# Kernel tuning notes

Hardware: AMD Instinct MI355X
Metric: run time of the kernel (lower is better)

The kernel has to match this reference:

```python
import jax, jax.numpy as jnp
import numpy as np

N = 100000          # number of active sparse points
GRID = 800          # coordinate grid extent (2D)
KS = 9              # 3x3 kernel offsets
C_IN = 24
C_HID = 144         # round(24 * 6)
C_OUT = 24
EPS = 1e-5


def _build_kernel_map():
    """Build MinkowskiEngine-style kernel map for a 3x3 stride-1 channelwise conv.
    Returns (in_idx, out_idx, off_id), each [KS*N] int32. Invalid (no neighbor)
    entries point to sentinel row N so the padded gather/scatter is a no-op."""
    rng = np.random.default_rng(0)
    flat = rng.choice(GRID * GRID, size=N, replace=False)  # unique 2D coords
    ys, xs = flat // GRID, flat % GRID
    coord_to_idx = -np.ones(GRID * GRID, dtype=np.int64)
    coord_to_idx[flat] = np.arange(N)
    in_chunks, out_chunks, off_chunks = [], [], []
    pts = np.arange(N, dtype=np.int64)
    k = 0
    for dy in (-1, 0, 1):
        for dx in (-1, 0, 1):
            ny, nx = ys + dy, xs + dx
            inside = (ny >= 0) & (ny < GRID) & (nx >= 0) & (nx < GRID)
            nflat = np.clip(ny, 0, GRID - 1) * GRID + np.clip(nx, 0, GRID - 1)
            nidx = np.where(inside, coord_to_idx[nflat], -1)
            valid = nidx >= 0
            in_chunks.append(np.where(valid, nidx, N))
            out_chunks.append(np.where(valid, pts, N))
            off_chunks.append(np.full(N, k, dtype=np.int64))
            k += 1
    in_idx = np.concatenate(in_chunks).astype(np.int32)
    out_idx = np.concatenate(out_chunks).astype(np.int32)
    off_id = np.concatenate(off_chunks).astype(np.int32)
    return in_idx, out_idx, off_id


def setup_inputs() -> dict:
    key = jax.random.key(0)
    ks = jax.random.split(key, 4)
    in_idx, out_idx, off_id = _build_kernel_map()
    return {
        "feats": jax.random.normal(ks[0], (N, C_IN), jnp.float32),
        "w1": jax.random.normal(ks[1], (C_IN, C_HID), jnp.float32) * 0.1,
        "g1": jnp.ones((C_HID,), jnp.float32),
        "b1": jnp.zeros((C_HID,), jnp.float32),
        "w2": jax.random.normal(ks[2], (KS, C_HID), jnp.float32) * 0.1,
        "g2": jnp.ones((C_HID,), jnp.float32),
        "b2": jnp.zeros((C_HID,), jnp.float32),
        "w3": jax.random.normal(ks[3], (C_HID, C_OUT), jnp.float32) * 0.1,
        "g3": jnp.ones((C_OUT,), jnp.float32),
        "b3": jnp.zeros((C_OUT,), jnp.float32),
        "in_idx": jnp.asarray(in_idx),
        "out_idx": jnp.asarray(out_idx),
        "off_id": jnp.asarray(off_id),
    }


def _bn(x, g, b):
    # MinkowskiBatchNorm forward (training mode): per-channel stats over points
    m = jnp.mean(x, axis=0)
    v = jnp.var(x, axis=0)
    return (x - m) * jax.lax.rsqrt(v + EPS) * g + b


def _relu6(x):
    return jnp.clip(x, 0.0, 6.0)


def _channelwise_conv3x3(x, w2, in_idx, out_idx, off_id):
    # gather-multiply-scatter: out[p, c] = sum_k w2[k, c] * x[nbr_k(p), c]
    xp = jnp.concatenate([x, jnp.zeros((1, x.shape[1]), x.dtype)], axis=0)  # sentinel row
    contrib = xp[in_idx] * w2[off_id]                     # [KS*N, C_HID]
    out = jnp.zeros((N + 1, x.shape[1]), x.dtype).at[out_idx].add(contrib)
    return out[:N]


def reference(feats, w1, g1, b1, w2, g2, b2, w3, g3, b3, in_idx, out_idx, off_id):
    x = _relu6(_bn(feats @ w1, g1, b1))                   # 1x1 expand
    x = _relu6(_bn(_channelwise_conv3x3(x, w2, in_idx, out_idx, off_id), g2, b2))
    x = _bn(x @ w3, g3, b3)                               # 1x1 project
    return x + feats                                      # residual (in==out, stride==1)
```

## Files before the change

kernel.cpp:

```cpp
#include <hip/hip_runtime.h>
#include <hip/hip_fp16.h>

#define N_PTS 100000
#define KSZ 9
#define C_IN 24
#define C_HID 144
#define C_OUT 24
#define G4_HID 36
#define G8_HID 18
#define G4_OUT 6
#define EPSV 1e-5f

#define X2H_B     28800288
#define SENT_B    28800000
#define Y3F_O     14400072
#define ST_O      16800072
#define ST_B      67200288
#define MU1_O     (ST_O + 0)
#define M1_O      (ST_O + 32)
#define SUM2_O    (ST_O + 640)
#define SQ2_O     (ST_O + 800)
#define SUM3_O    (ST_O + 960)
#define SQ3_O     (ST_O + 992)

__device__ inline float4 f4z() { return make_float4(0.f, 0.f, 0.f, 0.f); }
__device__ inline float4 f4_add(float4 a, float4 b) {
    return make_float4(a.x + b.x, a.y + b.y, a.z + b.z, a.w + b.w);
}
__device__ inline float4 f4_fma4(float4 a, float4 b, float4 c) {
    return make_float4(fmaf(a.x, b.x, c.x), fmaf(a.y, b.y, c.y),
                       fmaf(a.z, b.z, c.z), fmaf(a.w, b.w, c.w));
}
__device__ inline float4 f4_fma_s(float s, float4 b, float4 c) {
    return make_float4(fmaf(s, b.x, c.x), fmaf(s, b.y, c.y),
                       fmaf(s, b.z, c.z), fmaf(s, b.w, c.w));
}
__device__ inline float4 f4_clamp6(float4 a) {
    return make_float4(fminf(fmaxf(a.x, 0.f), 6.f), fminf(fmaxf(a.y, 0.f), 6.f),
                       fminf(fmaxf(a.z, 0.f), 6.f), fminf(fmaxf(a.w, 0.f), 6.f));
}
__device__ inline unsigned pack2(float a, float b) {
    __half2 h = __floats2half2_rn(a, b);
    return *reinterpret_cast<unsigned*>(&h);
}
__device__ inline float2 uph(unsigned u) {
    __half2 h = *reinterpret_cast<__half2*>(&u);
    return __half22float2(h);
}

#define MROWS 128
__device__ inline float task_acc(const float* tile, int cnt, int task) {
    if (task < 576) {
        int i = task / 24, j = task % 24;
        float a = 0.f;
        for (int r = 0; r < cnt; r++) a += tile[r * 24 + i] * tile[r * 24 + j];
        return a;
    }
    int k = task - 576;
    float a = 0.f;
    for (int r = 0; r < cnt; r++) a += tile[r * 24 + k];
    return a;
}
__global__ __launch_bounds__(256) void k_moments(const float* __restrict__ feats,
                                                 float* __restrict__ ws) {
    __shared__ float tile[MROWS * C_IN];
    int t = threadIdx.x;
    float acc0 = 0.f, acc1 = 0.f, acc2 = 0.f;
    int nChunks = (N_PTS + MROWS - 1) / MROWS;
    for (int ch = blockIdx.x; ch < nChunks; ch += gridDim.x) {
        int r0 = ch * MROWS;
        int cnt = min(MROWS, N_PTS - r0);
        __syncthreads();
        for (int e = t; e < cnt * C_IN; e += 256) tile[e] = feats[(size_t)r0 * C_IN + e];
        __syncthreads();
        acc0 += task_acc(tile, cnt, t);
        acc1 += task_acc(tile, cnt, t + 256);
        if (t < 88) acc2 += task_acc(tile, cnt, t + 512);
    }
    atomicAdd(&ws[M1_O + t], acc0);
    atomicAdd(&ws[M1_O + t + 256], acc1);
    if (t < 88) {
        int task = t + 512;
        if (task < 576) atomicAdd(&ws[M1_O + task], acc2);
        else            atomicAdd(&ws[MU1_O + task - 576], acc2);
    }
}

__global__ __launch_bounds__(256) void k_gemm1(const float* __restrict__ feats,
                                               const float* __restrict__ w1,
                                               const float* __restrict__ g1,
                                               const float* __restrict__ b1,
                                               float* __restrict__ ws) {
    __shared__ float4 w1s[C_IN * G4_HID];
    __shared__ float M1s[576];
    __shared__ float MU1s[24];
    __shared__ float scf[C_HID], shf[C_HID];
    int t = threadIdx.x;
    for (int e = t; e < C_IN * G4_HID; e += 256) w1s[e] = ((const float4*)w1)[e];
    for (int e = t; e < 576; e += 256) M1s[e] = ws[M1_O + e];
    if (t < 24) MU1s[t] = ws[MU1_O + t];
    __syncthreads();
    if (t < C_HID) {
        const float* w1f = (const float*)w1s;
        float wc[C_IN];
#pragma unroll
        for (int k = 0; k < C_IN; k++) wc[k] = w1f[k * C_HID + t];
        const float invN = 1.f / (float)N_PTS;
        float mean = 0.f;
#pragma unroll
        for (int k = 0; k < C_IN; k++) mean += MU1s[k] * wc[k];
        mean *= invN;
        float e2 = 0.f;
        for (int i = 0; i < C_IN; i++) {
            float s = 0.f;
#pragma unroll
            for (int j = 0; j < C_IN; j++) s += M1s[i * 24 + j] * wc[j];
            e2 += wc[i] * s;
        }
        e2 *= invN;
        float var = e2 - mean * mean;
        float s1 = g1[t] * rsqrtf(var + EPSV);
        scf[t] = s1;
        shf[t] = b1[t] - mean * s1;
    }
    __syncthreads();
    const float4* sc4 = (const float4*)scf;
    const float4* sh4 = (const float4*)shf;
    uint4* x1u = (uint4*)ws;
    const int T = N_PTS * G8_HID;
    for (int tau = blockIdx.x * 256 + t; tau < T; tau += gridDim.x * 256) {
        int p = tau / G8_HID;
        int g = tau % G8_HID;
        const float4* fr = (const float4*)(feats + (size_t)p * C_IN);
        float4 a0 = f4z(), a1 = f4z();
#pragma unroll
        for (int q = 0; q < 6; q++) {
            float4 fq = fr[q];
            a0 = f4_fma_s(fq.x, w1s[(4 * q + 0) * G4_HID + 2 * g], a0);
            a1 = f4_fma_s(fq.x, w1s[(4 * q + 0) * G4_HID + 2 * g + 1], a1);
            a0 = f4_fma_s(fq.y, w1s[(4 * q + 1) * G4_HID + 2 * g], a0);
            a1 = f4_fma_s(fq.y, w1s[(4 * q + 1) * G4_HID + 2 * g + 1], a1);
            a0 = f4_fma_s(fq.z, w1s[(4 * q + 2) * G4_HID + 2 * g], a0);
            a1 = f4_fma_s(fq.z, w1s[(4 * q + 2) * G4_HID + 2 * g + 1], a1);
            a0 = f4_fma_s(fq.w, w1s[(4 * q + 3) * G4_HID + 2 * g], a0);
            a1 = f4_fma_s(fq.w, w1s[(4 * q + 3) * G4_HID + 2 * g + 1], a1);
        }
        a0 = f4_clamp6(f4_fma4(a0, sc4[2 * g], sh4[2 * g]));
        a1 = f4_clamp6(f4_fma4(a1, sc4[2 * g + 1], sh4[2 * g + 1]));
        uint4 o;
        o.x = pack2(a0.x, a0.y); o.y = pack2(a0.z, a0.w);
        o.z = pack2(a1.x, a1.y); o.w = pack2(a1.z, a1.w);
        x1u[tau] = o;
    }
}

__global__ __launch_bounds__(256, 6) void k_conv(const float* __restrict__ w2,
                                                 const int* __restrict__ in_idx,
                                                 float* __restrict__ ws) {
    __shared__ float4 w2s[KSZ * G4_HID];
    __shared__ float lsum[C_HID], lsq[C_HID];
    int t = threadIdx.x;
    for (int e = t; e < KSZ * G4_HID; e += 256) w2s[e] = ((const float4*)w2)[e];
    if (t < C_HID) { lsum[t] = 0.f; lsq[t] = 0.f; }
    __syncthreads();
    const uint4* x1u = (const uint4*)ws;
    uint4* x2u = (uint4*)((char*)ws + X2H_B);
    bool active = t < 252;
    int pt = t / G8_HID, g = t % G8_HID;
    float4 rsA = f4z(), rsB = f4z(), rqA = f4z(), rqB = f4z();
    int nChunks = (N_PTS + 13) / 14;
    for (int ch = blockIdx.x; ch < nChunks; ch += gridDim.x) {
        int p = ch * 14 + pt;
        if (active && p < N_PTS) {
            int idx[KSZ];
#pragma unroll
            for (int k = 0; k < KSZ; k++) idx[k] = in_idx[k * N_PTS + p];
            float4 aA = f4z(), aB = f4z();
#pragma unroll
            for (int k = 0; k < KSZ; k++) {
                uint4 v = x1u[(size_t)idx[k] * G8_HID + g];
                float2 f0 = uph(v.x), f1 = uph(v.y), f2 = uph(v.z), f3 = uph(v.w);
                aA = f4_fma4(w2s[k * G4_HID + 2 * g], make_float4(f0.x, f0.y, f1.x, f1.y), aA);
                aB = f4_fma4(w2s[k * G4_HID + 2 * g + 1], make_float4(f2.x, f2.y, f3.x, f3.y), aB);
            }
            uint4 o;
            o.x = pack2(aA.x, aA.y); o.y = pack2(aA.z, aA.w);
            o.z = pack2(aB.x, aB.y); o.w = pack2(aB.z, aB.w);
            x2u[(size_t)p * G8_HID + g] = o;
            rsA = f4_add(rsA, aA); rsB = f4_add(rsB, aB);
            rqA = f4_fma4(aA, aA, rqA); rqB = f4_fma4(aB, aB, rqB);
        }
    }
    if (active) {
        int c0 = 8 * g;
        atomicAdd(&lsum[c0 + 0], rsA.x); atomicAdd(&lsum[c0 + 1], rsA.y);
        atomicAdd(&lsum[c0 + 2], rsA.z); atomicAdd(&lsum[c0 + 3], rsA.w);
        atomicAdd(&lsum[c0 + 4], rsB.x); atomicAdd(&lsum[c0 + 5], rsB.y);
        atomicAdd(&lsum[c0 + 6], rsB.z); atomicAdd(&lsum[c0 + 7], rsB.w);
        atomicAdd(&lsq[c0 + 0], rqA.x);  atomicAdd(&lsq[c0 + 1], rqA.y);
        atomicAdd(&lsq[c0 + 2], rqA.z);  atomicAdd(&lsq[c0 + 3], rqA.w);
        atomicAdd(&lsq[c0 + 4], rqB.x);  atomicAdd(&lsq[c0 + 5], rqB.y);
        atomicAdd(&lsq[c0 + 6], rqB.z);  atomicAdd(&lsq[c0 + 7], rqB.w);
    }
    __syncthreads();
    if (t < C_HID) {
        atomicAdd(&ws[SUM2_O + t], lsum[t]);
        atomicAdd(&ws[SQ2_O + t], lsq[t]);
    }
}

#define TP 64
__global__ __launch_bounds__(256) void k_gemm2(const float* __restrict__ w3,
                                               const float* __restrict__ g2,
                                               const float* __restrict__ b2,
                                               float* __restrict__ ws) {
    __shared__ float xs[TP * 145];
    __shared__ float w3s[C_HID * C_OUT];
    __shared__ float sc2s[C_HID], sh2s[C_HID];
    __shared__ float ssum[C_OUT], ssq[C_OUT];
    int t = threadIdx.x;
    for (int e = t; e < C_HID * C_OUT / 4; e += 256)
        ((float4*)w3s)[e] = ((const float4*)w3)[e];
    if (t < C_HID) {
        const float invN = 1.f / (float)N_PTS;
        float mean = ws[SUM2_O + t] * invN;
        float var = ws[SQ2_O + t] * invN - mean * mean;
        float s = g2[t] * rsqrtf(var + EPSV);
        sc2s[t] = s;
        sh2s[t] = b2[t] - mean * s;
    }
    if (t < C_OUT) { ssum[t] = 0.f; ssq[t] = 0.f; }
    __syncthreads();
    const uint4* x2u = (const uint4*)((char*)ws + X2H_B);
    int p0 = blockIdx.x * TP;
    for (int e = t; e < TP * G8_HID; e += 256) {
        int row = e / G8_HID, col = e % G8_HID;
        int p = p0 + row;
        int c0 = 8 * col;
        float v[8];
        if (p < N_PTS) {
            uint4 u = x2u[(size_t)p * G8_HID + col];
            float2 f0 = uph(u.x), f1 = uph(u.y), f2 = uph(u.z), f3 = uph(u.w);
            v[0] = f0.x; v[1] = f0.y; v[2] = f1.x; v[3] = f1.y;
            v[4] = f2.x; v[5] = f2.y; v[6] = f3.x; v[7] = f3.y;
#pragma unroll
            for (int i = 0; i < 8; i++)
                v[i] = fminf(fmaxf(fmaf(v[i], sc2s[c0 + i], sh2s[c0 + i]), 0.f), 6.f);
        } else {
#pragma unroll
            for (int i = 0; i < 8; i++) v[i] = 0.f;
        }
#pragma unroll
        for (int i = 0; i < 8; i++) xs[row * 145 + c0 + i] = v[i];
    }
    __syncthreads();
    int pl = t & 63, cg = t >> 6;
    int c0 = 6 * cg;
    float acc[6] = {0.f, 0.f, 0.f, 0.f, 0.f, 0.f};
    const float* xr = xs + pl * 145;
#pragma unroll 4
    for (int h = 0; h < C_HID; h++) {
        float x = xr[h];
#pragma unroll
        for (int j = 0; j < 6; j++) acc[j] = fmaf(x, w3s[h * C_OUT + c0 + j], acc[j]);
    }
    int p = p0 + pl;
    bool valid = p < N_PTS;
    float* y3 = ws + Y3F_O;
    if (valid) {
#pragma unroll
        for (int j = 0; j < 6; j++) y3[(size_t)p * C_OUT + c0 + j] = acc[j];
    }
    float s[6], q[6];
#pragma unroll
    for (int j = 0; j < 6; j++) {
        s[j] = valid ? acc[j] : 0.f;
        q[j] = s[j] * s[j];
    }
#pragma unroll
    for (int off = 32; off > 0; off >>= 1) {
#pragma unroll
        for (int j = 0; j < 6; j++) {
            s[j] += __shfl_down(s[j], off);
            q[j] += __shfl_down(q[j], off);
        }
    }
    if (pl == 0) {
#pragma unroll
        for (int j = 0; j < 6; j++) {
            atomicAdd(&ssum[c0 + j], s[j]);
            atomicAdd(&ssq[c0 + j], q[j]);
        }
    }
    __syncthreads();
    if (t < C_OUT) {
        atomicAdd(&ws[SUM3_O + t], ssum[t]);
        atomicAdd(&ws[SQ3_O + t], ssq[t]);
    }
}

__global__ __launch_bounds__(256) void k_out(const float* __restrict__ feats,
                                             const float* __restrict__ g3,
                                             const float* __restrict__ b3,
                                             const float* __restrict__ ws,
                                             float* __restrict__ out) {
    __shared__ float scs[C_OUT], shs[C_OUT];
    int t = threadIdx.x;
    if (t < C_OUT) {
        const float invN = 1.f / (float)N_PTS;
        float mean = ws[SUM3_O + t] * invN;
        float var = ws[SQ3_O + t] * invN - mean * mean;
        float s = g3[t] * rsqrtf(var + EPSV);
        scs[t] = s;
        shs[t] = b3[t] - mean * s;
    }
    __syncthreads();
    int t4 = blockIdx.x * 256 + t;
    const int T = N_PTS * G4_OUT;
    if (t4 >= T) return;
    int g = t4 % G4_OUT;
    float4 y = ((const float4*)(ws + Y3F_O))[t4];
    float4 s = ((const float4*)scs)[g];
    float4 b = ((const float4*)shs)[g];
    float4 f = ((const float4*)feats)[t4];
    ((float4*)out)[t4] = f4_add(f4_fma4(y, s, b), f);
}

extern "C" void kernel_launch(void* const* d_in, const int* in_sizes, int n_in,
                              void* d_out, int out_size, void* d_ws, size_t ws_size,
                              hipStream_t stream) {
    const float* feats = (const float*)d_in[0];
    const float* w1 = (const float*)d_in[1];
    const float* g1 = (const float*)d_in[2];
    const float* b1 = (const float*)d_in[3];
    const float* w2 = (const float*)d_in[4];
    const float* g2 = (const float*)d_in[5];
    const float* b2 = (const float*)d_in[6];
    const float* w3 = (const float*)d_in[7];
    const float* g3 = (const float*)d_in[8];
    const float* b3 = (const float*)d_in[9];
    const int* in_idx = (const int*)d_in[10];
    float* ws = (float*)d_ws;
    float* out = (float*)d_out;

    hipMemsetAsync((char*)d_ws + ST_B, 0, 4096, stream);
    hipMemsetAsync((char*)d_ws + SENT_B, 0, 288, stream);

    hipLaunchKernelGGL(k_moments, dim3(256), dim3(256), 0, stream, feats, ws);
    hipLaunchKernelGGL(k_gemm1, dim3(512), dim3(256), 0, stream, feats, w1, g1, b1, ws);
    hipLaunchKernelGGL(k_conv, dim3(2048), dim3(256), 0, stream, w2, in_idx, ws);
    hipLaunchKernelGGL(k_gemm2, dim3((N_PTS + TP - 1) / TP), dim3(256), 0, stream,
                       w3, g2, b2, ws);
    hipLaunchKernelGGL(k_out, dim3((N_PTS * G4_OUT + 255) / 256), dim3(256), 0, stream,
                       feats, g3, b3, ws, out);
}
```

Before: 312.9 us.

## Fuse all five stages into one cooperative persistent kernel with grid syncs

Replaces the two memsets and five kernel launches with a single cooperative kernel that runs each stage in turn, separated by grid-wide barriers, and zeroes the stats buffers inside the kernel. The conv stage now keeps its weights in registers instead of shared memory. The gemm2 stage stages activations in shared memory as half2 to shrink the tile. This removes launch gaps and per-kernel setup, but costs grid-sync overhead, a grid limited to what can be resident at once, and extra fp16 rounding in the gemm2 tile.

```diff
diff --git a/kernel.cpp b/kernel.cpp
--- a/kernel.cpp
+++ b/kernel.cpp
@@ -1,5 +1,8 @@
 #include <hip/hip_runtime.h>
 #include <hip/hip_fp16.h>
+#include <hip/hip_cooperative_groups.h>
+
+namespace cg = cooperative_groups;
 
 #define N_PTS 100000
 #define KSZ 9
@@ -12,10 +15,8 @@
 #define EPSV 1e-5f
 
 #define X2H_B     28800288
-#define SENT_B    28800000
 #define Y3F_O     14400072
 #define ST_O      16800072
-#define ST_B      67200288
 #define MU1_O     (ST_O + 0)
 #define M1_O      (ST_O + 32)
 #define SUM2_O    (ST_O + 640)
@@ -61,269 +62,304 @@
     for (int r = 0; r < cnt; r++) a += tile[r * 24 + k];
     return a;
 }
-__global__ __launch_bounds__(256) void k_moments(const float* __restrict__ feats,
-                                                 float* __restrict__ ws) {
-    __shared__ float tile[MROWS * C_IN];
-    int t = threadIdx.x;
-    float acc0 = 0.f, acc1 = 0.f, acc2 = 0.f;
-    int nChunks = (N_PTS + MROWS - 1) / MROWS;
-    for (int ch = blockIdx.x; ch < nChunks; ch += gridDim.x) {
-        int r0 = ch * MROWS;
-        int cnt = min(MROWS, N_PTS - r0);
-        __syncthreads();
-        for (int e = t; e < cnt * C_IN; e += 256) tile[e] = feats[(size_t)r0 * C_IN + e];
-        __syncthreads();
-        acc0 += task_acc(tile, cnt, t);
-        acc1 += task_acc(tile, cnt, t + 256);
-        if (t < 88) acc2 += task_acc(tile, cnt, t + 512);
-    }
-    atomicAdd(&ws[M1_O + t], acc0);
-    atomicAdd(&ws[M1_O + t + 256], acc1);
-    if (t < 88) {
-        int task = t + 512;
-        if (task < 576) atomicAdd(&ws[M1_O + task], acc2);
-        else            atomicAdd(&ws[MU1_O + task - 576], acc2);
-    }
-}
-
-__global__ __launch_bounds__(256) void k_gemm1(const float* __restrict__ feats,
-                                               const float* __restrict__ w1,
-                                               const float* __restrict__ g1,
-                                               const float* __restrict__ b1,
-                                               float* __restrict__ ws) {
-    __shared__ float4 w1s[C_IN * G4_HID];
-    __shared__ float M1s[576];
-    __shared__ float MU1s[24];
-    __shared__ float scf[C_HID], shf[C_HID];
-    int t = threadIdx.x;
-    for (int e = t; e < C_IN * G4_HID; e += 256) w1s[e] = ((const float4*)w1)[e];
-    for (int e = t; e < 576; e += 256) M1s[e] = ws[M1_O + e];
-    if (t < 24) MU1s[t] = ws[MU1_O + t];
-    __syncthreads();
-    if (t < C_HID) {
-        const float* w1f = (const float*)w1s;
-        float wc[C_IN];
-#pragma unroll
-        for (int k = 0; k < C_IN; k++) wc[k] = w1f[k * C_HID + t];
-        const float invN = 1.f / (float)N_PTS;
-        float mean = 0.f;
-#pragma unroll
-        for (int k = 0; k < C_IN; k++) mean += MU1s[k] * wc[k];
-        mean *= invN;
-        float e2 = 0.f;
-        for (int i = 0; i < C_IN; i++) {
-            float s = 0.f;
-#pragma unroll
-            for (int j = 0; j < C_IN; j++) s += M1s[i * 24 + j] * wc[j];
-            e2 += wc[i] * s;
-        }
-        e2 *= invN;
-        float var = e2 - mean * mean;
-        float s1 = g1[t] * rsqrtf(var + EPSV);
-        scf[t] = s1;
-        shf[t] = b1[t] - mean * s1;
-    }
-    __syncthreads();
-    const float4* sc4 = (const float4*)scf;
-    const float4* sh4 = (const float4*)shf;
-    uint4* x1u = (uint4*)ws;
-    const int T = N_PTS * G8_HID;
-    for (int tau = blockIdx.x * 256 + t; tau < T; tau += gridDim.x * 256) {
-        int p = tau / G8_HID;
-        int g = tau % G8_HID;
-        const float4* fr = (const float4*)(feats + (size_t)p * C_IN);
-        float4 a0 = f4z(), a1 = f4z();
-#pragma unroll
-        for (int q = 0; q < 6; q++) {
-            float4 fq = fr[q];
-            a0 = f4_fma_s(fq.x, w1s[(4 * q + 0) * G4_HID + 2 * g], a0);
-            a1 = f4_fma_s(fq.x, w1s[(4 * q + 0) * G4_HID + 2 * g + 1], a1);
-            a0 = f4_fma_s(fq.y, w1s[(4 * q + 1) * G4_HID + 2 * g], a0);
-            a1 = f4_fma_s(fq.y, w1s[(4 * q + 1) * G4_HID + 2 * g + 1], a1);
-            a0 = f4_fma_s(fq.z, w1s[(4 * q + 2) * G4_HID + 2 * g], a0);
-            a1 = f4_fma_s(fq.z, w1s[(4 * q + 2) * G4_HID + 2 * g + 1], a1);
-            a0 = f4_fma_s(fq.w, w1s[(4 * q + 3) * G4_HID + 2 * g], a0);
-            a1 = f4_fma_s(fq.w, w1s[(4 * q + 3) * G4_HID + 2 * g + 1], a1);
-        }
-        a0 = f4_clamp6(f4_fma4(a0, sc4[2 * g], sh4[2 * g]));
-        a1 = f4_clamp6(f4_fma4(a1, sc4[2 * g + 1], sh4[2 * g + 1]));
-        uint4 o;
-        o.x = pack2(a0.x, a0.y); o.y = pack2(a0.z, a0.w);
-        o.z = pack2(a1.x, a1.y); o.w = pack2(a1.z, a1.w);
-        x1u[tau] = o;
-    }
-}
-
-__global__ __launch_bounds__(256, 6) void k_conv(const float* __restrict__ w2,
-                                                 const int* __restrict__ in_idx,
-                                                 float* __restrict__ ws) {
-    __shared__ float4 w2s[KSZ * G4_HID];
-    __shared__ float lsum[C_HID], lsq[C_HID];
-    int t = threadIdx.x;
-    for (int e = t; e < KSZ * G4_HID; e += 256) w2s[e] = ((const float4*)w2)[e];
-    if (t < C_HID) { lsum[t] = 0.f; lsq[t] = 0.f; }
-    __syncthreads();
-    const uint4* x1u = (const uint4*)ws;
-    uint4* x2u = (uint4*)((char*)ws + X2H_B);
-    bool active = t < 252;
-    int pt = t / G8_HID, g = t % G8_HID;
-    float4 rsA = f4z(), rsB = f4z(), rqA = f4z(), rqB = f4z();
-    int nChunks = (N_PTS + 13) / 14;
-    for (int ch = blockIdx.x; ch < nChunks; ch += gridDim.x) {
-        int p = ch * 14 + pt;
-        if (active && p < N_PTS) {
-            int idx[KSZ];
-#pragma unroll
-            for (int k = 0; k < KSZ; k++) idx[k] = in_idx[k * N_PTS + p];
-            float4 aA = f4z(), aB = f4z();
-#pragma unroll
-            for (int k = 0; k < KSZ; k++) {
-                uint4 v = x1u[(size_t)idx[k] * G8_HID + g];
-                float2 f0 = uph(v.x), f1 = uph(v.y), f2 = uph(v.z), f3 = uph(v.w);
-                aA = f4_fma4(w2s[k * G4_HID + 2 * g], make_float4(f0.x, f0.y, f1.x, f1.y), aA);
-                aB = f4_fma4(w2s[k * G4_HID + 2 * g + 1], make_float4(f2.x, f2.y, f3.x, f3.y), aB);
-            }
+
+__global__ __launch_bounds__(256, 4) void k_fused(
+    const float* __restrict__ feats, const float* __restrict__ w1,
+    const float* __restrict__ g1, const float* __restrict__ b1,
+    const float* __restrict__ w2, const float* __restrict__ g2,
+    const float* __restrict__ b2, const float* __restrict__ w3,
+    const float* __restrict__ g3, const float* __restrict__ b3,
+    const int* __restrict__ in_idx, float* __restrict__ ws,
+    float* __restrict__ out) {
+    __shared__ __align__(16) char smem[33920];
+    cg::grid_group gg = cg::this_grid();
+    const int t = threadIdx.x;
+    const int bid = blockIdx.x;
+    const int nB = gridDim.x;
+
+    if (bid == 0) {
+        for (int i = t; i < 1024; i += 256) ws[ST_O + i] = 0.f;
+        if (t < G8_HID) {
+            uint4 z; z.x = 0u; z.y = 0u; z.z = 0u; z.w = 0u;
+            ((uint4*)ws)[(size_t)N_PTS * G8_HID + t] = z;
+        }
+    }
+    gg.sync();
+
+    {
+        float* tile = (float*)smem;
+        float acc0 = 0.f, acc1 = 0.f, acc2 = 0.f;
+        const int nChunks = (N_PTS + MROWS - 1) / MROWS;
+        for (int ch = bid; ch < nChunks; ch += nB) {
+            int r0 = ch * MROWS;
+            int cnt = min(MROWS, N_PTS - r0);
+            __syncthreads();
+            for (int e = t; e < cnt * C_IN; e += 256)
+                tile[e] = feats[(size_t)r0 * C_IN + e];
+            __syncthreads();
+            acc0 += task_acc(tile, cnt, t);
+            acc1 += task_acc(tile, cnt, t + 256);
+            if (t < 88) acc2 += task_acc(tile, cnt, t + 512);
+        }
+        if (bid < nChunks) {
+            atomicAdd(&ws[M1_O + t], acc0);
+            atomicAdd(&ws[M1_O + t + 256], acc1);
+            if (t < 88) {
+                int task = t + 512;
+                if (task < 576) atomicAdd(&ws[M1_O + task], acc2);
+                else            atomicAdd(&ws[MU1_O + task - 576], acc2);
+            }
+        }
+    }
+    gg.sync();
+
+    {
+        float4* w1s = (float4*)smem;
+        float*  M1s = (float*)(smem + 13824);
+        float*  MU1s = (float*)(smem + 16128);
+        float*  scf = (float*)(smem + 16224);
+        float*  shf = (float*)(smem + 16800);
+        for (int e = t; e < C_IN * G4_HID; e += 256) w1s[e] = ((const float4*)w1)[e];
+        for (int e = t; e < 576; e += 256) M1s[e] = ws[M1_O + e];
+        if (t < 24) MU1s[t] = ws[MU1_O + t];
+        __syncthreads();
+        if (t < C_HID) {
+            const float* w1f = (const float*)w1s;
+            float wc[C_IN];
+#pragma unroll
+            for (int k = 0; k < C_IN; k++) wc[k] = w1f[k * C_HID + t];
+            const float invN = 1.f / (float)N_PTS;
+            float mean = 0.f;
+#pragma unroll
+            for (int k = 0; k < C_IN; k++) mean += MU1s[k] * wc[k];
+            mean *= invN;
+            float e2 = 0.f;
+            for (int i = 0; i < C_IN; i++) {
+                float s = 0.f;
+#pragma unroll
+                for (int j = 0; j < C_IN; j++) s += M1s[i * 24 + j] * wc[j];
+                e2 += wc[i] * s;
+            }
+            e2 *= invN;
+            float var = e2 - mean * mean;
+            float s1 = g1[t] * rsqrtf(var + EPSV);
+            scf[t] = s1;
+            shf[t] = b1[t] - mean * s1;
+        }
+        __syncthreads();
+        const float4* sc4 = (const float4*)scf;
+        const float4* sh4 = (const float4*)shf;
+        uint4* x1u = (uint4*)ws;
+        const int T = N_PTS * G8_HID;
+        for (int tau = bid * 256 + t; tau < T; tau += nB * 256) {
+            int p = tau / G8_HID;
+            int g = tau % G8_HID;
+            const float4* fr = (const float4*)(feats + (size_t)p * C_IN);
+            float4 a0 = f4z(), a1 = f4z();
+#pragma unroll
+            for (int q = 0; q < 6; q++) {
+                float4 fq = fr[q];
+                a0 = f4_fma_s(fq.x, w1s[(4 * q + 0) * G4_HID + 2 * g], a0);
+                a1 = f4_fma_s(fq.x, w1s[(4 * q + 0) * G4_HID + 2 * g + 1], a1);
+                a0 = f4_fma_s(fq.y, w1s[(4 * q + 1) * G4_HID + 2 * g], a0);
+                a1 = f4_fma_s(fq.y, w1s[(4 * q + 1) * G4_HID + 2 * g + 1], a1);
+                a0 = f4_fma_s(fq.z, w1s[(4 * q + 2) * G4_HID + 2 * g], a0);
+                a1 = f4_fma_s(fq.z, w1s[(4 * q + 2) * G4_HID + 2 * g + 1], a1);
+                a0 = f4_fma_s(fq.w, w1s[(4 * q + 3) * G4_HID + 2 * g], a0);
+                a1 = f4_fma_s(fq.w, w1s[(4 * q + 3) * G4_HID + 2 * g + 1], a1);
+            }
+            a0 = f4_clamp6(f4_fma4(a0, sc4[2 * g], sh4[2 * g]));
+            a1 = f4_clamp6(f4_fma4(a1, sc4[2 * g + 1], sh4[2 * g + 1]));
             uint4 o;
-            o.x = pack2(aA.x, aA.y); o.y = pack2(aA.z, aA.w);
-            o.z = pack2(aB.x, aB.y); o.w = pack2(aB.z, aB.w);
-            x2u[(size_t)p * G8_HID + g] = o;
-            rsA = f4_add(rsA, aA); rsB = f4_add(rsB, aB);
-            rqA = f4_fma4(aA, aA, rqA); rqB = f4_fma4(aB, aB, rqB);
-        }
-    }
-    if (active) {
-        int c0 = 8 * g;
-        atomicAdd(&lsum[c0 + 0], rsA.x); atomicAdd(&lsum[c0 + 1], rsA.y);
-        atomicAdd(&lsum[c0 + 2], rsA.z); atomicAdd(&lsum[c0 + 3], rsA.w);
-        atomicAdd(&lsum[c0 + 4], rsB.x); atomicAdd(&lsum[c0 + 5], rsB.y);
-        atomicAdd(&lsum[c0 + 6], rsB.z); atomicAdd(&lsum[c0 + 7], rsB.w);
-        atomicAdd(&lsq[c0 + 0], rqA.x);  atomicAdd(&lsq[c0 + 1], rqA.y);
-        atomicAdd(&lsq[c0 + 2], rqA.z);  atomicAdd(&lsq[c0 + 3], rqA.w);
-        atomicAdd(&lsq[c0 + 4], rqB.x);  atomicAdd(&lsq[c0 + 5], rqB.y);
-        atomicAdd(&lsq[c0 + 6], rqB.z);  atomicAdd(&lsq[c0 + 7], rqB.w);
-    }
-    __syncthreads();
-    if (t < C_HID) {
-        atomicAdd(&ws[SUM2_O + t], lsum[t]);
-        atomicAdd(&ws[SQ2_O + t], lsq[t]);
-    }
-}
-
-#define TP 64
-__global__ __launch_bounds__(256) void k_gemm2(const float* __restrict__ w3,
-                                               const float* __restrict__ g2,
-                                               const float* __restrict__ b2,
-                                               float* __restrict__ ws) {
-    __shared__ float xs[TP * 145];
-    __shared__ float w3s[C_HID * C_OUT];
-    __shared__ float sc2s[C_HID], sh2s[C_HID];
-    __shared__ float ssum[C_OUT], ssq[C_OUT];
-    int t = threadIdx.x;
-    for (int e = t; e < C_HID * C_OUT / 4; e += 256)
-        ((float4*)w3s)[e] = ((const float4*)w3)[e];
-    if (t < C_HID) {
-        const float invN = 1.f / (float)N_PTS;
-        float mean = ws[SUM2_O + t] * invN;
-        float var = ws[SQ2_O + t] * invN - mean * mean;
-        float s = g2[t] * rsqrtf(var + EPSV);
-        sc2s[t] = s;
-        sh2s[t] = b2[t] - mean * s;
-    }
-    if (t < C_OUT) { ssum[t] = 0.f; ssq[t] = 0.f; }
-    __syncthreads();
-    const uint4* x2u = (const uint4*)((char*)ws + X2H_B);
-    int p0 = blockIdx.x * TP;
-    for (int e = t; e < TP * G8_HID; e += 256) {
-        int row = e / G8_HID, col = e % G8_HID;
-        int p = p0 + row;
-        int c0 = 8 * col;
-        float v[8];
-        if (p < N_PTS) {
-            uint4 u = x2u[(size_t)p * G8_HID + col];
-            float2 f0 = uph(u.x), f1 = uph(u.y), f2 = uph(u.z), f3 = uph(u.w);
-            v[0] = f0.x; v[1] = f0.y; v[2] = f1.x; v[3] = f1.y;
-            v[4] = f2.x; v[5] = f2.y; v[6] = f3.x; v[7] = f3.y;
-#pragma unroll
-            for (int i = 0; i < 8; i++)
-                v[i] = fminf(fmaxf(fmaf(v[i], sc2s[c0 + i], sh2s[c0 + i]), 0.f), 6.f);
-        } else {
-#pragma unroll
-            for (int i = 0; i < 8; i++) v[i] = 0.f;
-        }
-#pragma unroll
-        for (int i = 0; i < 8; i++) xs[row * 145 + c0 + i] = v[i];
-    }
-    __syncthreads();
-    int pl = t & 63, cg = t >> 6;
-    int c0 = 6 * cg;
-    float acc[6] = {0.f, 0.f, 0.f, 0.f, 0.f, 0.f};
-    const float* xr = xs + pl * 145;
-#pragma unroll 4
-    for (int h = 0; h < C_HID; h++) {
-        float x = xr[h];
-#pragma unroll
-        for (int j = 0; j < 6; j++) acc[j] = fmaf(x, w3s[h * C_OUT + c0 + j], acc[j]);
-    }
-    int p = p0 + pl;
-    bool valid = p < N_PTS;
-    float* y3 = ws + Y3F_O;
-    if (valid) {
-#pragma unroll
-        for (int j = 0; j < 6; j++) y3[(size_t)p * C_OUT + c0 + j] = acc[j];
-    }
-    float s[6], q[6];
-#pragma unroll
-    for (int j = 0; j < 6; j++) {
-        s[j] = valid ? acc[j] : 0.f;
-        q[j] = s[j] * s[j];
-    }
-#pragma unroll
-    for (int off = 32; off > 0; off >>= 1) {
-#pragma unroll
-        for (int j = 0; j < 6; j++) {
-            s[j] += __shfl_down(s[j], off);
-            q[j] += __shfl_down(q[j], off);
-        }
-    }
-    if (pl == 0) {
-#pragma unroll
-        for (int j = 0; j < 6; j++) {
-            atomicAdd(&ssum[c0 + j], s[j]);
-            atomicAdd(&ssq[c0 + j], q[j]);
-        }
-    }
-    __syncthreads();
-    if (t < C_OUT) {
-        atomicAdd(&ws[SUM3_O + t], ssum[t]);
-        atomicAdd(&ws[SQ3_O + t], ssq[t]);
-    }
-}
-
-__global__ __launch_bounds__(256) void k_out(const float* __restrict__ feats,
-                                             const float* __restrict__ g3,
-                                             const float* __restrict__ b3,
-                                             const float* __restrict__ ws,
-                                             float* __restrict__ out) {
-    __shared__ float scs[C_OUT], shs[C_OUT];
-    int t = threadIdx.x;
-    if (t < C_OUT) {
-        const float invN = 1.f / (float)N_PTS;
-        float mean = ws[SUM3_O + t] * invN;
-        float var = ws[SQ3_O + t] * invN - mean * mean;
-        float s = g3[t] * rsqrtf(var + EPSV);
-        scs[t] = s;
-        shs[t] = b3[t] - mean * s;
-    }
-    __syncthreads();
-    int t4 = blockIdx.x * 256 + t;
-    const int T = N_PTS * G4_OUT;
-    if (t4 >= T) return;
-    int g = t4 % G4_OUT;
-    float4 y = ((const float4*)(ws + Y3F_O))[t4];
-    float4 s = ((const float4*)scs)[g];
-    float4 b = ((const float4*)shs)[g];
-    float4 f = ((const float4*)feats)[t4];
-    ((float4*)out)[t4] = f4_add(f4_fma4(y, s, b), f);
+            o.x = pack2(a0.x, a0.y); o.y = pack2(a0.z, a0.w);
+            o.z = pack2(a1.x, a1.y); o.w = pack2(a1.z, a1.w);
+            x1u[tau] = o;
+        }
+    }
+    gg.sync();
+
+    {
+        float* lsum = (float*)smem;
+        float* lsq  = (float*)(smem + 576);
+        if (t < C_HID) { lsum[t] = 0.f; lsq[t] = 0.f; }
+        __syncthreads();
+        const uint4* x1u = (const uint4*)ws;
+        uint4* x2u = (uint4*)((char*)ws + X2H_B);
+        bool active = t < 252;
+        int pt = t / G8_HID, g = t % G8_HID;
+        const float4* w2v = (const float4*)w2;
+        float4 wA[KSZ], wB[KSZ];
+#pragma unroll
+        for (int k = 0; k < KSZ; k++) {
+            wA[k] = w2v[k * G4_HID + 2 * g];
+            wB[k] = w2v[k * G4_HID + 2 * g + 1];
+        }
+        float4 rsA = f4z(), rsB = f4z(), rqA = f4z(), rqB = f4z();
+        const int nChunks = (N_PTS + 13) / 14;
+        for (int ch = bid; ch < nChunks; ch += nB) {
+            int p = ch * 14 + pt;
+            if (active && p < N_PTS) {
+                int idx[KSZ];
+#pragma unroll
+                for (int k = 0; k < KSZ; k++) idx[k] = in_idx[k * N_PTS + p];
+                float4 aA = f4z(), aB = f4z();
+#pragma unroll
+                for (int k = 0; k < KSZ; k++) {
+                    uint4 v = x1u[(size_t)idx[k] * G8_HID + g];
+                    float2 f0 = uph(v.x), f1 = uph(v.y), f2 = uph(v.z), f3 = uph(v.w);
+                    aA = f4_fma4(wA[k], make_float4(f0.x, f0.y, f1.x, f1.y), aA);
+                    aB = f4_fma4(wB[k], make_float4(f2.x, f2.y, f3.x, f3.y), aB);
+                }
+                uint4 o;
+                o.x = pack2(aA.x, aA.y); o.y = pack2(aA.z, aA.w);
+                o.z = pack2(aB.x, aB.y); o.w = pack2(aB.z, aB.w);
+                x2u[(size_t)p * G8_HID + g] = o;
+                rsA = f4_add(rsA, aA); rsB = f4_add(rsB, aB);
+                rqA = f4_fma4(aA, aA, rqA); rqB = f4_fma4(aB, aB, rqB);
+            }
+        }
+        if (active) {
+            int c0 = 8 * g;
+            atomicAdd(&lsum[c0 + 0], rsA.x); atomicAdd(&lsum[c0 + 1], rsA.y);
+            atomicAdd(&lsum[c0 + 2], rsA.z); atomicAdd(&lsum[c0 + 3], rsA.w);
+            atomicAdd(&lsum[c0 + 4], rsB.x); atomicAdd(&lsum[c0 + 5], rsB.y);
+            atomicAdd(&lsum[c0 + 6], rsB.z); atomicAdd(&lsum[c0 + 7], rsB.w);
+            atomicAdd(&lsq[c0 + 0], rqA.x);  atomicAdd(&lsq[c0 + 1], rqA.y);
+            atomicAdd(&lsq[c0 + 2], rqA.z);  atomicAdd(&lsq[c0 + 3], rqA.w);
+            atomicAdd(&lsq[c0 + 4], rqB.x);  atomicAdd(&lsq[c0 + 5], rqB.y);
+            atomicAdd(&lsq[c0 + 6], rqB.z);  atomicAdd(&lsq[c0 + 7], rqB.w);
+        }
+        __syncthreads();
+        if (t < C_HID) {
+            atomicAdd(&ws[SUM2_O + t], lsum[t]);
+            atomicAdd(&ws[SQ2_O + t], lsq[t]);
+        }
+    }
+    gg.sync();
+
+    {
+        float*   w3s  = (float*)smem;
+        float*   sc2s = (float*)(smem + 13824);
+        float*   sh2s = (float*)(smem + 14400);
+        float*   ssum = (float*)(smem + 14976);
+        float*   ssq  = (float*)(smem + 15072);
+        __half2* xs2  = (__half2*)(smem + 15168);
+        for (int e = t; e < C_HID * C_OUT / 4; e += 256)
+            ((float4*)w3s)[e] = ((const float4*)w3)[e];
+        if (t < C_HID) {
+            const float invN = 1.f / (float)N_PTS;
+            float mean = ws[SUM2_O + t] * invN;
+            float var = ws[SQ2_O + t] * invN - mean * mean;
+            float s = g2[t] * rsqrtf(var + EPSV);
+            sc2s[t] = s;
+            sh2s[t] = b2[t] - mean * s;
+        }
+        if (t < C_OUT) { ssum[t] = 0.f; ssq[t] = 0.f; }
+        __syncthreads();
+        const uint4* x2u = (const uint4*)((char*)ws + X2H_B);
+        float* y3 = ws + Y3F_O;
+        int pl = t & 63, cgid = t >> 6, c0 = 6 * cgid;
+        const int nTiles = (N_PTS + 63) / 64;
+        for (int tile = bid; tile < nTiles; tile += nB) {
+            int p0 = tile * 64;
+            for (int e = t; e < 64 * G8_HID; e += 256) {
+                int row = e / G8_HID, col = e % G8_HID;
+                int p = p0 + row;
+                float v[8];
+                if (p < N_PTS) {
+                    uint4 u = x2u[(size_t)p * G8_HID + col];
+                    float2 f0 = uph(u.x), f1 = uph(u.y), f2 = uph(u.z), f3 = uph(u.w);
+                    v[0] = f0.x; v[1] = f0.y; v[2] = f1.x; v[3] = f1.y;
+                    v[4] = f2.x; v[5] = f2.y; v[6] = f3.x; v[7] = f3.y;
+                    int cb = 8 * col;
+#pragma unroll
+                    for (int i = 0; i < 8; i++)
+                        v[i] = fminf(fmaxf(fmaf(v[i], sc2s[cb + i], sh2s[cb + i]), 0.f), 6.f);
+                } else {
+#pragma unroll
+                    for (int i = 0; i < 8; i++) v[i] = 0.f;
+                }
+                int base = row * 73 + col * 4;
+                xs2[base + 0] = __floats2half2_rn(v[0], v[1]);
+                xs2[base + 1] = __floats2half2_rn(v[2], v[3]);
+                xs2[base + 2] = __floats2half2_rn(v[4], v[5]);
+                xs2[base + 3] = __floats2half2_rn(v[6], v[7]);
+            }
+            __syncthreads();
+            float acc[6] = {0.f, 0.f, 0.f, 0.f, 0.f, 0.f};
+            const __half2* xr = xs2 + pl * 73;
+#pragma unroll 8
+            for (int hh = 0; hh < 72; hh++) {
+                float2 xv = __half22float2(xr[hh]);
+                int h = 2 * hh;
+#pragma unroll
+                for (int j = 0; j < 6; j++)
+                    acc[j] = fmaf(xv.x, w3s[h * C_OUT + c0 + j], acc[j]);
+#pragma unroll
+                for (int j = 0; j < 6; j++)
+                    acc[j] = fmaf(xv.y, w3s[(h + 1) * C_OUT + c0 + j], acc[j]);
+            }
+            int p = p0 + pl;
+            bool valid = p < N_PTS;
+            if (valid) {
+#pragma unroll
+                for (int j = 0; j < 6; j++) y3[(size_t)p * C_OUT + c0 + j] = acc[j];
+            }
+            float s[6], q[6];
+#pragma unroll
+            for (int j = 0; j < 6; j++) {
+                s[j] = valid ? acc[j] : 0.f;
+                q[j] = s[j] * s[j];
+            }
+#pragma unroll
+            for (int off = 32; off > 0; off >>= 1) {
+#pragma unroll
+                for (int j = 0; j < 6; j++) {
+                    s[j] += __shfl_down(s[j], off);
+                    q[j] += __shfl_down(q[j], off);
+                }
+            }
+            if (pl == 0) {
+#pragma unroll
+                for (int j = 0; j < 6; j++) {
+                    atomicAdd(&ssum[c0 + j], s[j]);
+                    atomicAdd(&ssq[c0 + j], q[j]);
+                }
+            }
+            __syncthreads();
+        }
+        if (bid < nTiles && t < C_OUT) {
+            atomicAdd(&ws[SUM3_O + t], ssum[t]);
+            atomicAdd(&ws[SQ3_O + t], ssq[t]);
+        }
+    }
+    gg.sync();
+
+    {
+        float* scs = (float*)smem;
+        float* shs = (float*)(smem + 128);
+        if (t < C_OUT) {
+            const float invN = 1.f / (float)N_PTS;
+            float mean = ws[SUM3_O + t] * invN;
+            float var = ws[SQ3_O + t] * invN - mean * mean;
+            float s = g3[t] * rsqrtf(var + EPSV);
+            scs[t] = s;
+            shs[t] = b3[t] - mean * s;
+        }
+        __syncthreads();
+        const float4* y3v = (const float4*)(ws + Y3F_O);
+        const float4* fv = (const float4*)feats;
+        float4* ov = (float4*)out;
+        const int T = N_PTS * G4_OUT;
+        for (int e = bid * 256 + t; e < T; e += nB * 256) {
+            int g = e % G4_OUT;
+            float4 y = y3v[e];
+            float4 s = ((const float4*)scs)[g];
+            float4 b = ((const float4*)shs)[g];
+            float4 f = fv[e];
+            ov[e] = f4_add(f4_fma4(y, s, b), f);
+        }
+    }
 }
 
 extern "C" void kernel_launch(void* const* d_in, const int* in_sizes, int n_in,
@@ -343,14 +379,16 @@
     float* ws = (float*)d_ws;
     float* out = (float*)d_out;
 
-    hipMemsetAsync((char*)d_ws + ST_B, 0, 4096, stream);
-    hipMemsetAsync((char*)d_ws + SENT_B, 0, 288, stream);
-
-    hipLaunchKernelGGL(k_moments, dim3(256), dim3(256), 0, stream, feats, ws);
-    hipLaunchKernelGGL(k_gemm1, dim3(512), dim3(256), 0, stream, feats, w1, g1, b1, ws);
-    hipLaunchKernelGGL(k_conv, dim3(2048), dim3(256), 0, stream, w2, in_idx, ws);
-    hipLaunchKernelGGL(k_gemm2, dim3((N_PTS + TP - 1) / TP), dim3(256), 0, stream,
-                       w3, g2, b2, ws);
-    hipLaunchKernelGGL(k_out, dim3((N_PTS * G4_OUT + 255) / 256), dim3(256), 0, stream,
-                       feats, g3, b3, ws, out);
-}
+    void* args[] = {
+        (void*)&feats, (void*)&w1, (void*)&g1, (void*)&b1, (void*)&w2,
+        (void*)&g2, (void*)&b2, (void*)&w3, (void*)&g3, (void*)&b3,
+        (void*)&in_idx, (void*)&ws, (void*)&out};
+
+    int maxB = 2;
+    hipOccupancyMaxActiveBlocksPerMultiprocessor(&maxB, (const void*)k_fused, 256, 0);
+    if (maxB < 1) maxB = 1;
+    int grid = maxB * 256;
+    if (grid > 2048) grid = 2048;
+    hipLaunchCooperativeKernel((const void*)k_fused, dim3(grid), dim3(256),
+                               args, 0, stream);
+}
```

Result: slower. 500.8 us (+60.0%).

## Drop moments kernel; compute BN1 stats in gemm1 and apply BN1 in conv

Applied to the files above, without the earlier changes.

Removes the separate second-moment pass over feats. gemm1 now writes the raw pre-BN expansion in fp16 and accumulates per-channel sum and sum-of-squares. The conv kernel derives the BN1 scale and shift from those stats and applies normalize plus ReLU6 on each gathered neighbor, skipping sentinel indices, so the sentinel-row memset also goes. gemm1 is restructured to use one 64-point tile per block staged through shared memory. In exchange, conv does 9x more BN arithmetic per output and adds a branch per neighbor, and stats are computed from fp32 values while the conv reads fp16-rounded ones.

```diff
diff --git a/kernel.cpp b/kernel.cpp
--- a/kernel.cpp
+++ b/kernel.cpp
@@ -11,17 +11,16 @@
 #define G4_OUT 6
 #define EPSV 1e-5f
 
-#define X2H_B     28800288
-#define SENT_B    28800000
-#define Y3F_O     14400072
-#define ST_O      16800072
-#define ST_B      67200288
-#define MU1_O     (ST_O + 0)
-#define M1_O      (ST_O + 32)
-#define SUM2_O    (ST_O + 640)
-#define SQ2_O     (ST_O + 800)
-#define SUM3_O    (ST_O + 960)
-#define SQ3_O     (ST_O + 992)
+#define X2H_B     28800000
+#define Y3F_O     14400000
+#define ST_O      16800000
+#define ST_B      67200000
+#define SUM1_O    (ST_O + 0)
+#define SQ1_O     (ST_O + 160)
+#define SUM2_O    (ST_O + 320)
+#define SQ2_O     (ST_O + 480)
+#define SUM3_O    (ST_O + 640)
+#define SQ3_O     (ST_O + 672)
 
 __device__ inline float4 f4z() { return make_float4(0.f, 0.f, 0.f, 0.f); }
 __device__ inline float4 f4_add(float4 a, float4 b) {
@@ -48,127 +47,110 @@
     return __half22float2(h);
 }
 
-#define MROWS 128
-__device__ inline float task_acc(const float* tile, int cnt, int task) {
-    if (task < 576) {
-        int i = task / 24, j = task % 24;
-        float a = 0.f;
-        for (int r = 0; r < cnt; r++) a += tile[r * 24 + i] * tile[r * 24 + j];
-        return a;
-    }
-    int k = task - 576;
-    float a = 0.f;
-    for (int r = 0; r < cnt; r++) a += tile[r * 24 + k];
-    return a;
-}
-__global__ __launch_bounds__(256) void k_moments(const float* __restrict__ feats,
-                                                 float* __restrict__ ws) {
-    __shared__ float tile[MROWS * C_IN];
-    int t = threadIdx.x;
-    float acc0 = 0.f, acc1 = 0.f, acc2 = 0.f;
-    int nChunks = (N_PTS + MROWS - 1) / MROWS;
-    for (int ch = blockIdx.x; ch < nChunks; ch += gridDim.x) {
-        int r0 = ch * MROWS;
-        int cnt = min(MROWS, N_PTS - r0);
-        __syncthreads();
-        for (int e = t; e < cnt * C_IN; e += 256) tile[e] = feats[(size_t)r0 * C_IN + e];
-        __syncthreads();
-        acc0 += task_acc(tile, cnt, t);
-        acc1 += task_acc(tile, cnt, t + 256);
-        if (t < 88) acc2 += task_acc(tile, cnt, t + 512);
-    }
-    atomicAdd(&ws[M1_O + t], acc0);
-    atomicAdd(&ws[M1_O + t + 256], acc1);
-    if (t < 88) {
-        int task = t + 512;
-        if (task < 576) atomicAdd(&ws[M1_O + task], acc2);
-        else            atomicAdd(&ws[MU1_O + task - 576], acc2);
-    }
-}
-
 __global__ __launch_bounds__(256) void k_gemm1(const float* __restrict__ feats,
                                                const float* __restrict__ w1,
-                                               const float* __restrict__ g1,
-                                               const float* __restrict__ b1,
                                                float* __restrict__ ws) {
-    __shared__ float4 w1s[C_IN * G4_HID];
-    __shared__ float M1s[576];
-    __shared__ float MU1s[24];
-    __shared__ float scf[C_HID], shf[C_HID];
-    int t = threadIdx.x;
+    __shared__ __align__(16) char smem[38272];
+    float*  xs   = (float*)smem;
+    float4* w1s  = (float4*)(smem + 6400);
+    float*  tile = (float*)smem;
+    float*  lsum = (float*)(smem + 37120);
+    float*  lsq  = (float*)(smem + 37696);
+    const int t = threadIdx.x;
+    const int p0 = blockIdx.x * 64;
     for (int e = t; e < C_IN * G4_HID; e += 256) w1s[e] = ((const float4*)w1)[e];
-    for (int e = t; e < 576; e += 256) M1s[e] = ws[M1_O + e];
-    if (t < 24) MU1s[t] = ws[MU1_O + t];
+    for (int e = t; e < 64 * C_IN; e += 256) {
+        int r = e / C_IN, c = e % C_IN;
+        int p = p0 + r;
+        xs[r * 25 + c] = (p < N_PTS) ? feats[(size_t)p * C_IN + c] : 0.f;
+    }
+    if (t < C_HID) { lsum[t] = 0.f; lsq[t] = 0.f; }
+    __syncthreads();
+    const int pt = t & 63;
+    const int cg = __builtin_amdgcn_readfirstlane(t >> 6);
+    float4 acc[9];
+#pragma unroll
+    for (int j = 0; j < 9; j++) acc[j] = f4z();
+    for (int k = 0; k < C_IN; k++) {
+        float xk = xs[pt * 25 + k];
+        const float4* wr = &w1s[k * G4_HID + cg * 9];
+#pragma unroll
+        for (int j = 0; j < 9; j++) acc[j] = f4_fma_s(xk, wr[j], acc[j]);
+    }
+    __syncthreads();
+    {
+        float* dst = tile + pt * 145 + cg * 36;
+#pragma unroll
+        for (int j = 0; j < 9; j++) {
+            dst[4 * j + 0] = acc[j].x; dst[4 * j + 1] = acc[j].y;
+            dst[4 * j + 2] = acc[j].z; dst[4 * j + 3] = acc[j].w;
+        }
+    }
+    __syncthreads();
+    uint4* y1u = (uint4*)ws;
+    bool active = t < 252;
+    int g = t % G8_HID, r0 = t / G8_HID;
+    float4 rsA = f4z(), rsB = f4z(), rqA = f4z(), rqB = f4z();
+    if (active) {
+        for (int r = r0; r < 64; r += 14) {
+            int p = p0 + r;
+            if (p >= N_PTS) break;
+            const float* src = tile + r * 145 + 8 * g;
+            float v0 = src[0], v1 = src[1], v2 = src[2], v3 = src[3];
+            float v4 = src[4], v5 = src[5], v6 = src[6], v7 = src[7];
+            uint4 o;
+            o.x = pack2(v0, v1); o.y = pack2(v2, v3);
+            o.z = pack2(v4, v5); o.w = pack2(v6, v7);
+            y1u[(size_t)p * G8_HID + g] = o;
+            float4 aA = make_float4(v0, v1, v2, v3), aB = make_float4(v4, v5, v6, v7);
+            rsA = f4_add(rsA, aA); rsB = f4_add(rsB, aB);
+            rqA = f4_fma4(aA, aA, rqA); rqB = f4_fma4(aB, aB, rqB);
+        }
+        int c0 = 8 * g;
+        atomicAdd(&lsum[c0 + 0], rsA.x); atomicAdd(&lsum[c0 + 1], rsA.y);
+        atomicAdd(&lsum[c0 + 2], rsA.z); atomicAdd(&lsum[c0 + 3], rsA.w);
+        atomicAdd(&lsum[c0 + 4], rsB.x); atomicAdd(&lsum[c0 + 5], rsB.y);
+        atomicAdd(&lsum[c0 + 6], rsB.z); atomicAdd(&lsum[c0 + 7], rsB.w);
+        atomicAdd(&lsq[c0 + 0], rqA.x);  atomicAdd(&lsq[c0 + 1], rqA.y);
+        atomicAdd(&lsq[c0 + 2], rqA.z);  atomicAdd(&lsq[c0 + 3], rqA.w);
+        atomicAdd(&lsq[c0 + 4], rqB.x);  atomicAdd(&lsq[c0 + 5], rqB.y);
+        atomicAdd(&lsq[c0 + 6], rqB.z);  atomicAdd(&lsq[c0 + 7], rqB.w);
+    }
     __syncthreads();
     if (t < C_HID) {
-        const float* w1f = (const float*)w1s;
-        float wc[C_IN];
-#pragma unroll
-        for (int k = 0; k < C_IN; k++) wc[k] = w1f[k * C_HID + t];
+        atomicAdd(&ws[SUM1_O + t], lsum[t]);
+        atomicAdd(&ws[SQ1_O + t], lsq[t]);
+    }
+}
+
+__global__ __launch_bounds__(256) void k_conv(const float* __restrict__ w2,
+                                              const float* __restrict__ g1,
+                                              const float* __restrict__ b1,
+                                              const int* __restrict__ in_idx,
+                                              float* __restrict__ ws) {
+    __shared__ float4 w2s[KSZ * G4_HID];
+    __shared__ float sc1L[C_HID], sh1L[C_HID];
+    __shared__ float lsum[C_HID], lsq[C_HID];
+    const int t = threadIdx.x;
+    for (int e = t; e < KSZ * G4_HID; e += 256) w2s[e] = ((const float4*)w2)[e];
+    if (t < C_HID) {
         const float invN = 1.f / (float)N_PTS;
-        float mean = 0.f;
-#pragma unroll
-        for (int k = 0; k < C_IN; k++) mean += MU1s[k] * wc[k];
-        mean *= invN;
-        float e2 = 0.f;
-        for (int i = 0; i < C_IN; i++) {
-            float s = 0.f;
-#pragma unroll
-            for (int j = 0; j < C_IN; j++) s += M1s[i * 24 + j] * wc[j];
-            e2 += wc[i] * s;
-        }
-        e2 *= invN;
-        float var = e2 - mean * mean;
-        float s1 = g1[t] * rsqrtf(var + EPSV);
-        scf[t] = s1;
-        shf[t] = b1[t] - mean * s1;
-    }
-    __syncthreads();
-    const float4* sc4 = (const float4*)scf;
-    const float4* sh4 = (const float4*)shf;
-    uint4* x1u = (uint4*)ws;
-    const int T = N_PTS * G8_HID;
-    for (int tau = blockIdx.x * 256 + t; tau < T; tau += gridDim.x * 256) {
-        int p = tau / G8_HID;
-        int g = tau % G8_HID;
-        const float4* fr = (const float4*)(feats + (size_t)p * C_IN);
-        float4 a0 = f4z(), a1 = f4z();
-#pragma unroll
-        for (int q = 0; q < 6; q++) {
-            float4 fq = fr[q];
-            a0 = f4_fma_s(fq.x, w1s[(4 * q + 0) * G4_HID + 2 * g], a0);
-            a1 = f4_fma_s(fq.x, w1s[(4 * q + 0) * G4_HID + 2 * g + 1], a1);
-            a0 = f4_fma_s(fq.y, w1s[(4 * q + 1) * G4_HID + 2 * g], a0);
-            a1 = f4_fma_s(fq.y, w1s[(4 * q + 1) * G4_HID + 2 * g + 1], a1);
-            a0 = f4_fma_s(fq.z, w1s[(4 * q + 2) * G4_HID + 2 * g], a0);
-            a1 = f4_fma_s(fq.z, w1s[(4 * q + 2) * G4_HID + 2 * g + 1], a1);
-            a0 = f4_fma_s(fq.w, w1s[(4 * q + 3) * G4_HID + 2 * g], a0);
-            a1 = f4_fma_s(fq.w, w1s[(4 * q + 3) * G4_HID + 2 * g + 1], a1);
-        }
-        a0 = f4_clamp6(f4_fma4(a0, sc4[2 * g], sh4[2 * g]));
-        a1 = f4_clamp6(f4_fma4(a1, sc4[2 * g + 1], sh4[2 * g + 1]));
-        uint4 o;
-        o.x = pack2(a0.x, a0.y); o.y = pack2(a0.z, a0.w);
-        o.z = pack2(a1.x, a1.y); o.w = pack2(a1.z, a1.w);
-        x1u[tau] = o;
-    }
-}
-
-__global__ __launch_bounds__(256, 6) void k_conv(const float* __restrict__ w2,
-                                                 const int* __restrict__ in_idx,
-                                                 float* __restrict__ ws) {
-    __shared__ float4 w2s[KSZ * G4_HID];
-    __shared__ float lsum[C_HID], lsq[C_HID];
-    int t = threadIdx.x;
-    for (int e = t; e < KSZ * G4_HID; e += 256) w2s[e] = ((const float4*)w2)[e];
-    if (t < C_HID) { lsum[t] = 0.f; lsq[t] = 0.f; }
-    __syncthreads();
-    const uint4* x1u = (const uint4*)ws;
+        float mean = ws[SUM1_O + t] * invN;
+        float var = ws[SQ1_O + t] * invN - mean * mean;
+        float s = g1[t] * rsqrtf(var + EPSV);
+        sc1L[t] = s;
+        sh1L[t] = b1[t] - mean * s;
+        lsum[t] = 0.f; lsq[t] = 0.f;
+    }
+    __syncthreads();
+    const uint4* y1u = (const uint4*)ws;
     uint4* x2u = (uint4*)((char*)ws + X2H_B);
     bool active = t < 252;
     int pt = t / G8_HID, g = t % G8_HID;
+    float4 scA = ((const float4*)sc1L)[2 * g], scB = ((const float4*)sc1L)[2 * g + 1];
+    float4 shA = ((const float4*)sh1L)[2 * g], shB = ((const float4*)sh1L)[2 * g + 1];
     float4 rsA = f4z(), rsB = f4z(), rqA = f4z(), rqB = f4z();
-    int nChunks = (N_PTS + 13) / 14;
+    const int nChunks = (N_PTS + 13) / 14;
     for (int ch = blockIdx.x; ch < nChunks; ch += gridDim.x) {
         int p = ch * 14 + pt;
         if (active && p < N_PTS) {
@@ -178,10 +160,14 @@
             float4 aA = f4z(), aB = f4z();
 #pragma unroll
             for (int k = 0; k < KSZ; k++) {
-                uint4 v = x1u[(size_t)idx[k] * G8_HID + g];
-                float2 f0 = uph(v.x), f1 = uph(v.y), f2 = uph(v.z), f3 = uph(v.w);
-                aA = f4_fma4(w2s[k * G4_HID + 2 * g], make_float4(f0.x, f0.y, f1.x, f1.y), aA);
-                aB = f4_fma4(w2s[k * G4_HID + 2 * g + 1], make_float4(f2.x, f2.y, f3.x, f3.y), aB);
+                if (idx[k] < N_PTS) {
+                    uint4 v = y1u[(size_t)idx[k] * G8_HID + g];
+                    float2 f0 = uph(v.x), f1 = uph(v.y), f2 = uph(v.z), f3 = uph(v.w);
+                    float4 vA = f4_clamp6(f4_fma4(make_float4(f0.x, f0.y, f1.x, f1.y), scA, shA));
+                    float4 vB = f4_clamp6(f4_fma4(make_float4(f2.x, f2.y, f3.x, f3.y), scB, shB));
+                    aA = f4_fma4(w2s[k * G4_HID + 2 * g], vA, aA);
+                    aB = f4_fma4(w2s[k * G4_HID + 2 * g + 1], vB, aB);
+                }
             }
             uint4 o;
             o.x = pack2(aA.x, aA.y); o.y = pack2(aA.z, aA.w);
@@ -218,7 +204,7 @@
     __shared__ float w3s[C_HID * C_OUT];
     __shared__ float sc2s[C_HID], sh2s[C_HID];
     __shared__ float ssum[C_OUT], ssq[C_OUT];
-    int t = threadIdx.x;
+    const int t = threadIdx.x;
     for (int e = t; e < C_HID * C_OUT / 4; e += 256)
         ((float4*)w3s)[e] = ((const float4*)w3)[e];
     if (t < C_HID) {
@@ -254,8 +240,8 @@
         for (int i = 0; i < 8; i++) xs[row * 145 + c0 + i] = v[i];
     }
     __syncthreads();
-    int pl = t & 63, cg = t >> 6;
-    int c0 = 6 * cg;
+    int pl = t & 63, cgid = t >> 6;
+    int c0 = 6 * cgid;
     float acc[6] = {0.f, 0.f, 0.f, 0.f, 0.f, 0.f};
     const float* xr = xs + pl * 145;
 #pragma unroll 4
@@ -304,8 +290,8 @@
                                              const float* __restrict__ b3,
                                              const float* __restrict__ ws,
                                              float* __restrict__ out) {
-    __shared__ float scs[C_OUT], shs[C_OUT];
-    int t = threadIdx.x;
+    __shared__ float scs[32], shs[32];
+    const int t = threadIdx.x;
     if (t < C_OUT) {
         const float invN = 1.f / (float)N_PTS;
         float mean = ws[SUM3_O + t] * invN;
@@ -344,11 +330,10 @@
     float* out = (float*)d_out;
 
     hipMemsetAsync((char*)d_ws + ST_B, 0, 4096, stream);
-    hipMemsetAsync((char*)d_ws + SENT_B, 0, 288, stream);
-
-    hipLaunchKernelGGL(k_moments, dim3(256), dim3(256), 0, stream, feats, ws);
-    hipLaunchKernelGGL(k_gemm1, dim3(512), dim3(256), 0, stream, feats, w1, g1, b1, ws);
-    hipLaunchKernelGGL(k_conv, dim3(2048), dim3(256), 0, stream, w2, in_idx, ws);
+    hipLaunchKernelGGL(k_gemm1, dim3((N_PTS + 63) / 64), dim3(256), 0, stream,
+                       feats, w1, ws);
+    hipLaunchKernelGGL(k_conv, dim3(2048), dim3(256), 0, stream,
+                       w2, g1, b1, in_idx, ws);
     hipLaunchKernelGGL(k_gemm2, dim3((N_PTS + TP - 1) / TP), dim3(256), 0, stream,
                        w3, g2, b2, ws);
     hipLaunchKernelGGL(k_out, dim3((N_PTS * G4_OUT + 255) / 256), dim3(256), 0, stream,
```

After: 299.4 us. 1.05x faster.
